# Kernel tuning notes

Hardware: AMD Instinct MI355X
Metric: run time of the kernel (lower is better)

## Reference

```python
import jax, jax.numpy as jnp
import numpy as np

TOP_K = 2


def setup_inputs() -> dict:
    key = jax.random.key(0)
    ks = jax.random.split(key, 6)
    B, S, D, H, E = 2, 2048, 1024, 4096, 8
    s_in = 1.0 / np.sqrt(D)
    s_hid = 1.0 / np.sqrt(H)
    return {
        "x": jax.random.normal(ks[0], (B, S, D), jnp.float32),
        "Wg": jax.random.normal(ks[1], (E, D), jnp.float32) * s_in,
        "W1": jax.random.normal(ks[2], (E, D, H), jnp.float32) * s_in,
        "b1": jax.random.normal(ks[3], (E, H), jnp.float32) * 0.01,
        "W2": jax.random.normal(ks[4], (E, H, D), jnp.float32) * s_hid,
        "b2": jax.random.normal(ks[5], (E, D), jnp.float32) * 0.01,
    }


def reference(x, Wg, W1, b1, W2, b2):
    B, S, D = x.shape
    E = Wg.shape[0]
    T = B * S
    xf = x.reshape(T, D)

    # ---- router ----
    logits = xf @ Wg.T                              # (T, E)
    probs = jax.nn.softmax(logits, axis=-1)
    top_v, top_i = jax.lax.top_k(probs, TOP_K)      # (T, k)
    top_v = top_v / top_v.sum(axis=-1, keepdims=True)

    # aux load-balancing loss
    expert_mask = jax.nn.one_hot(top_i, E, dtype=probs.dtype).sum(axis=1)  # (T, E)
    f = expert_mask.mean(axis=0)
    p = probs.mean(axis=0)
    aux_loss = E * (f * p).sum()

    # ---- combine weights: scatter normalized top-k probs into (T, E) ----
    w = jnp.zeros((T, E), probs.dtype).at[jnp.arange(T)[:, None], top_i].add(top_v)

    # ---- all-expert FFN (grouped GEMM form), weighted combine ----
    h = jax.nn.silu(jnp.einsum('td,edh->teh', xf, W1) + b1[None])   # (T, E, H)
    y = jnp.einsum('teh,ehd->ted', h, W2) + b2[None]                # (T, E, D)
    out = jnp.einsum('ted,te->td', y, w)                            # (T, D)
    return out.reshape(B, S, D), aux_loss
```

## Files before the change

kernel.cpp:

```cpp
#include <hip/hip_runtime.h>
#include <cstdint>
#include <cstddef>

#define T_TOK 4096
#define DIM   1024
#define HID   4096
#define NE    8
#define PAD   128
#define PADMAX 9216
#define KSPLIT2 2

typedef _Float16 half_t;
typedef __attribute__((ext_vector_type(8))) _Float16 half8;
typedef __attribute__((ext_vector_type(4))) float floatx4;

__device__ __forceinline__ float silu_f(float v) {
  return v / (1.0f + expf(-v));
}

__device__ __forceinline__ half8 cvt44(float4 a, float4 b) {
  half8 o;
  o[0] = (half_t)a.x; o[1] = (half_t)a.y; o[2] = (half_t)a.z; o[3] = (half_t)a.w;
  o[4] = (half_t)b.x; o[5] = (half_t)b.y; o[6] = (half_t)b.z; o[7] = (half_t)b.w;
  return o;
}

__device__ __forceinline__ void gload16(const void* g, void* l) {
  __builtin_amdgcn_global_load_lds(
      (const __attribute__((address_space(1))) unsigned int*)g,
      (__attribute__((address_space(3))) unsigned int*)l, 16, 0, 0);
}

__device__ __forceinline__ int xcd_swz(int lin, int Nw) {
  int q = Nw >> 3;
  return (lin & 7) * q + (lin >> 3);
}


__device__ __forceinline__ void write_tiled(const half_t* sT, half_t* dstTile, int tid) {
#pragma unroll
  for (int t2 = 0; t2 < 4; ++t2) {
    int o = (t2 * 256 + tid) * 8;
    int m = o >> 9, p2 = o & 511;
    int lane2 = p2 >> 3;
    int rg = ((m >> 2) << 1) | ((m >> 1) & 1);
    int khalf = m & 1;
    int fr = rg * 16 + (lane2 & 15);
    int fk = khalf * 32 + (lane2 >> 4) * 8;
    half8 v;
#pragma unroll
    for (int j = 0; j < 8; ++j) v[j] = sT[(fk + j) * 136 + fr];
    *(half8*)(dstTile + o) = v;
  }
}

__global__ void k_reset(float* prob_sum, unsigned* cnt, unsigned* cursor,
                        int* pair_tok, float* pair_wt) {
  int i = blockIdx.x * 256 + threadIdx.x;
  if (i < PADMAX) { pair_tok[i] = 0; pair_wt[i] = 0.0f; }
  if (i < NE) { prob_sum[i] = 0.0f; cnt[i] = 0u; cursor[i] = 0u; }
}

__global__ __launch_bounds__(256) void k_cvt_x(const float* __restrict__ x,
                                               half_t* __restrict__ xh) {
  size_t i = (size_t)blockIdx.x * 256 + threadIdx.x;
  const float4* s = (const float4*)(x + i * 8);
  float4 a = s[0], b = s[1];
  *(half8*)(xh + i * 8) = cvt44(a, b);
}

__global__ __launch_bounds__(256) void k_tr_w1(const float* __restrict__ W1,
                                               half_t* __restrict__ W1c,
                                               int j0, int Hc) {
  __shared__ half_t sT[64 * 136];
  int e = blockIdx.z, J = blockIdx.x, Kd = blockIdx.y;
  int tid = threadIdx.x;
  {
    int rr = tid >> 2, q = tid & 3;
    const float* s = W1 + ((size_t)e * DIM + Kd * 64 + rr) * HID + j0 + J * 128 + q * 32;
    float4 f[8];
#pragma unroll
    for (int i = 0; i < 8; ++i) f[i] = ((const float4*)s)[i];
    half_t* d = sT + rr * 136 + q * 32;
#pragma unroll
    for (int i = 0; i < 4; ++i) *(half8*)(d + i * 8) = cvt44(f[2 * i], f[2 * i + 1]);
  }
  __syncthreads();
  half_t* dstTile = W1c + (((size_t)e * (Hc >> 7) + J) * (DIM / 64) + Kd) * 8192;
  write_tiled(sT, dstTile, tid);
}

__global__ __launch_bounds__(256) void k_tr_w2(const float* __restrict__ W2,
                                               half_t* __restrict__ W2c,
                                               int j0, int Hc) {
  __shared__ half_t sT[64 * 136];
  int e = blockIdx.z, J = blockIdx.x, K2 = blockIdx.y;
  int tid = threadIdx.x;
  {
    int hh = tid >> 2, q = tid & 3;
    const float* s = W2 + ((size_t)e * HID + j0 + K2 * 64 + hh) * DIM + J * 128 + q * 32;
    float4 f[8];
#pragma unroll
    for (int i = 0; i < 8; ++i) f[i] = ((const float4*)s)[i];
    half_t* d = sT + hh * 136 + q * 32;
#pragma unroll
    for (int i = 0; i < 4; ++i) *(half8*)(d + i * 8) = cvt44(f[2 * i], f[2 * i + 1]);
  }
  __syncthreads();
  half_t* dstTile = W2c + (((size_t)e * (DIM / 128) + J) * (Hc >> 6) + K2) * 8192;
  write_tiled(sT, dstTile, tid);
}

__global__ __launch_bounds__(256) void k_router(
    const float* __restrict__ x, const float* __restrict__ Wg,
    int* __restrict__ top_i, float* __restrict__ top_w,
    float* __restrict__ prob_sum, unsigned* __restrict__ cnt) {
  __shared__ float sWg[NE * DIM];
  __shared__ float sProb[NE];
  __shared__ unsigned sCnt[NE];
  int tid = threadIdx.x;
  if (tid < NE) { sProb[tid] = 0.0f; sCnt[tid] = 0u; }
  for (int i = tid; i < NE * DIM; i += 256) sWg[i] = Wg[i];
  __syncthreads();

  int wave = tid >> 6, lane = tid & 63;
  for (int it = 0; it < 4; ++it) {
    int t = blockIdx.x * 16 + wave * 4 + it;
    const float* xp = x + (size_t)t * DIM;
    float acc[NE];
#pragma unroll
    for (int e = 0; e < NE; ++e) acc[e] = 0.0f;
    for (int i = 0; i < DIM / 64; ++i) {
      int d = i * 64 + lane;
      float xd = xp[d];
#pragma unroll
      for (int e = 0; e < NE; ++e) acc[e] = fmaf(xd, sWg[e * DIM + d], acc[e]);
    }
#pragma unroll
    for (int off = 32; off > 0; off >>= 1)
#pragma unroll
      for (int e = 0; e < NE; ++e) acc[e] += __shfl_xor(acc[e], off, 64);

    if (lane == 0) {
      float m = acc[0];
#pragma unroll
      for (int e = 1; e < NE; ++e) m = fmaxf(m, acc[e]);
      float pr[NE]; float s = 0.0f;
#pragma unroll
      for (int e = 0; e < NE; ++e) { pr[e] = expf(acc[e] - m); s += pr[e]; }
      float inv = 1.0f / s;
#pragma unroll
      for (int e = 0; e < NE; ++e) pr[e] *= inv;
      int i0 = 0; float v0 = pr[0];
#pragma unroll
      for (int e = 1; e < NE; ++e) if (pr[e] > v0) { v0 = pr[e]; i0 = e; }
      int i1 = -1; float v1 = -1.0f;
#pragma unroll
      for (int e = 0; e < NE; ++e) if (e != i0 && pr[e] > v1) { v1 = pr[e]; i1 = e; }
      float wn = 1.0f / (v0 + v1);
      top_i[t * 2 + 0] = i0; top_i[t * 2 + 1] = i1;
      top_w[t * 2 + 0] = v0 * wn; top_w[t * 2 + 1] = v1 * wn;
#pragma unroll
      for (int e = 0; e < NE; ++e) atomicAdd(&sProb[e], pr[e]);
      atomicAdd(&sCnt[i0], 1u);
      atomicAdd(&sCnt[i1], 1u);
    }
  }
  __syncthreads();
  if (tid < NE) {
    atomicAdd(&prob_sum[tid], sProb[tid]);
    atomicAdd(&cnt[tid], sCnt[tid]);
  }
}

__global__ void k_scan(const unsigned* __restrict__ cnt,
                       const float* __restrict__ prob_sum,
                       int* __restrict__ pad_off, int* __restrict__ ptotal,
                       float* __restrict__ aux_out) {
  if (threadIdx.x == 0 && blockIdx.x == 0) {
    int off = 0; float aux = 0.0f;
    for (int e = 0; e < NE; ++e) {
      pad_off[e] = off;
      off += (int)((cnt[e] + (PAD - 1u)) & ~(unsigned)(PAD - 1));
      aux += ((float)cnt[e] / (float)T_TOK) * (prob_sum[e] / (float)T_TOK);
    }
    pad_off[NE] = off;
    *ptotal = off;
    *aux_out = (float)NE * aux;
  }
}

__global__ void k_scatter(const int* __restrict__ top_i, const float* __restrict__ top_w,
                          const int* __restrict__ pad_off, unsigned* __restrict__ cursor,
                          int* __restrict__ pair_tok, float* __restrict__ pair_wt) {
  int t = blockIdx.x * 256 + threadIdx.x;
  if (t >= T_TOK) return;
#pragma unroll
  for (int k = 0; k < 2; ++k) {
    int e = top_i[t * 2 + k];
    unsigned pos = atomicAdd(&cursor[e], 1u);
    int idx = pad_off[e] + (int)pos;
    pair_tok[idx] = t;
    pair_wt[idx]  = top_w[t * 2 + k];
  }
}

__global__ void k_init_out(const int* __restrict__ top_i, const float* __restrict__ top_w,
                           const float* __restrict__ b2, float* __restrict__ out) {
  int idx = blockIdx.x * 256 + threadIdx.x;
  int t = idx >> 10, d = idx & (DIM - 1);
  int e0 = top_i[t * 2 + 0], e1 = top_i[t * 2 + 1];
  out[idx] = top_w[t * 2 + 0] * b2[e0 * DIM + d] + top_w[t * 2 + 1] * b2[e1 * DIM + d];
}

__global__ __launch_bounds__(256) void k_gemm1_a(
    const half_t* __restrict__ xh, const half_t* __restrict__ W1c,
    const float* __restrict__ b1, const int* __restrict__ pair_tok,
    const int* __restrict__ pad_off, const int* __restrict__ ptotal,
    half_t* __restrict__ hbuf, int j0, int Hc) {
  __shared__ half_t lds[16384];
  int wid = xcd_swz(blockIdx.x, gridDim.x);
  int col = wid / (PADMAX / 128);
  int row = wid % (PADMAX / 128);
  int P = *ptotal;
  int p0 = row * 128;
  if (p0 >= P) return;
  int e = 0;
#pragma unroll
  for (int q = 1; q < NE; ++q) if (p0 >= pad_off[q]) e = q;

  int tid = threadIdx.x, w = tid >> 6, l = tid & 63;
  int lr = l & 15, lq = l >> 4;
  int wr = w >> 1, wc = w & 1;
  int w4 = 4 * w;
  int jt = col * 128;

  int tok0 = pair_tok[p0 + (2 * w) * 16 + lr];
  int tok1 = pair_tok[p0 + (2 * w + 1) * 16 + lr];
  const half_t* gA0 = xh + (size_t)tok0 * DIM + lq * 8;
  const half_t* gA1 = xh + (size_t)tok1 * DIM + lq * 8;
  const half_t* gBt = W1c + (((size_t)e * (Hc >> 7) + (jt >> 7)) * (DIM / 64)) * 8192 + l * 8;

  half_t* ldsA = lds;
  half_t* ldsB = lds + 8192;
  half_t* dA = ldsA + w4 * 512;
  half_t* dB = ldsB + w4 * 512;

  floatx4 acc[4][4];
#pragma unroll
  for (int i = 0; i < 4; ++i)
#pragma unroll
    for (int j = 0; j < 4; ++j) acc[i][j] = (floatx4){0.f, 0.f, 0.f, 0.f};

  for (int s = 0; s < DIM / 64; ++s) {
    int kt = s * 64;
    __syncthreads();
    gload16(gA0 + kt,      dA + 0 * 512);
    gload16(gA0 + kt + 32, dA + 1 * 512);
    gload16(gA1 + kt,      dA + 2 * 512);
    gload16(gA1 + kt + 32, dA + 3 * 512);
    const half_t* gBs = gBt + (size_t)s * 8192;
#pragma unroll
    for (int i = 0; i < 4; ++i) gload16(gBs + (w4 + i) * 512, dB + i * 512);
    __syncthreads();
#pragma unroll
    for (int ks = 0; ks < 2; ++ks) {
      half8 a[4], b[4];
#pragma unroll
      for (int i = 0; i < 4; ++i)
        a[i] = *(const half8*)(ldsA + ((4 * wr + i) * 2 + ks) * 512 + l * 8);
#pragma unroll
      for (int j = 0; j < 4; ++j)
        b[j] = *(const half8*)(ldsB + ((4 * wc + j) * 2 + ks) * 512 + l * 8);
#pragma unroll
      for (int i = 0; i < 4; ++i)
#pragma unroll
        for (int j = 0; j < 4; ++j)
          acc[i][j] = __builtin_amdgcn_mfma_f32_16x16x32_f16(a[i], b[j], acc[i][j], 0, 0, 0);
    }
  }
  __syncthreads();

#pragma unroll
  for (int j = 0; j < 4; ++j) {
    int coll = (4 * wc + j) * 16 + lr;
    float bias = b1[(size_t)e * HID + j0 + jt + coll];
#pragma unroll
    for (int i = 0; i < 4; ++i)
#pragma unroll
      for (int r = 0; r < 4; ++r) {
        int row2 = (4 * wr + i) * 16 + lq * 4 + r;
        lds[row2 * 128 + coll] = (half_t)silu_f(acc[i][j][r] + bias);
      }
  }
  __syncthreads();
  {
    size_t tb = ((size_t)(p0 >> 7) * (Hc >> 6) + (jt >> 6)) * 8192;
#pragma unroll
    for (int t2 = 0; t2 < 8; ++t2) {
      int o = (t2 * 256 + tid) * 8;
      int kk = o >> 13, rem = o & 8191;
      int m = rem >> 9, p2 = rem & 511;
      int lane2 = p2 >> 3;
      int rg = ((m >> 2) << 1) | ((m >> 1) & 1);
      int rr = rg * 16 + (lane2 & 15);
      int colb = kk * 64 + (m & 1) * 32 + (lane2 >> 4) * 8;
      *(half8*)(hbuf + tb + o) = *(const half8*)(lds + rr * 128 + colb);
    }
  }
}

__global__ __launch_bounds__(256) void k_gemm2_a(
    const half_t* __restrict__ hbuf, const half_t* __restrict__ W2c,
    const int* __restrict__ pair_tok, const float* __restrict__ pair_wt,
    const int* __restrict__ pad_off, const int* __restrict__ ptotal,
    float* __restrict__ out, int Hc) {
  __shared__ half_t lds[16384];
  int wid = xcd_swz(blockIdx.x, gridDim.x);
  int c  = wid & 7;
  int rz = wid >> 3;
  int row = rz % (PADMAX / 128);
  int zk  = rz / (PADMAX / 128);
  int P = *ptotal;
  int p0 = row * 128;
  if (p0 >= P) return;
  int e = 0;
#pragma unroll
  for (int q = 1; q < NE; ++q) if (p0 >= pad_off[q]) e = q;

  int tid = threadIdx.x, w = tid >> 6, l = tid & 63;
  int lr = l & 15, lq = l >> 4;
  int wr = w >> 1, wc = w & 1;
  int w4 = 4 * w;
  int jt = c * 128;

  int nkt = Hc >> 6;
  int t_beg = (zk * nkt) / KSPLIT2;
  int t_end = ((zk + 1) * nkt) / KSPLIT2;

  const half_t* gA = hbuf + ((size_t)row * nkt) * 8192 + l * 8;
  const half_t* gB = W2c + (((size_t)e * (DIM / 128) + c) * nkt) * 8192 + l * 8;

  half_t* ldsA = lds;
  half_t* ldsB = lds + 8192;
  half_t* dA = ldsA + w4 * 512;
  half_t* dB = ldsB + w4 * 512;

  floatx4 acc[4][4];
#pragma unroll
  for (int i = 0; i < 4; ++i)
#pragma unroll
    for (int j = 0; j < 4; ++j) acc[i][j] = (floatx4){0.f, 0.f, 0.f, 0.f};

  for (int s = t_beg; s < t_end; ++s) {
    const half_t* gAs = gA + (size_t)s * 8192;
    const half_t* gBs = gB + (size_t)s * 8192;
    __syncthreads();
#pragma unroll
    for (int i = 0; i < 4; ++i) gload16(gAs + (w4 + i) * 512, dA + i * 512);
#pragma unroll
    for (int i = 0; i < 4; ++i) gload16(gBs + (w4 + i) * 512, dB + i * 512);
    __syncthreads();
#pragma unroll
    for (int ks = 0; ks < 2; ++ks) {
      half8 a[4], b[4];
#pragma unroll
      for (int i = 0; i < 4; ++i)
        a[i] = *(const half8*)(ldsA + ((4 * wr + i) * 2 + ks) * 512 + l * 8);
#pragma unroll
      for (int j = 0; j < 4; ++j)
        b[j] = *(const half8*)(ldsB + ((4 * wc + j) * 2 + ks) * 512 + l * 8);
#pragma unroll
      for (int i = 0; i < 4; ++i)
#pragma unroll
        for (int j = 0; j < 4; ++j)
          acc[i][j] = __builtin_amdgcn_mfma_f32_16x16x32_f16(a[i], b[j], acc[i][j], 0, 0, 0);
    }
  }

#pragma unroll
  for (int i = 0; i < 4; ++i)
#pragma unroll
    for (int r = 0; r < 4; ++r) {
      int row2 = (4 * wr + i) * 16 + lq * 4 + r;
      float wt = pair_wt[p0 + row2];
      if (wt != 0.0f) {
        int tok = pair_tok[p0 + row2];
        float* op = out + (size_t)tok * DIM + jt;
#pragma unroll
        for (int j = 0; j < 4; ++j) {
          int coll = (4 * wc + j) * 16 + lr;
          unsafeAtomicAdd(op + coll, wt * acc[i][j][r]);
        }
      }
    }
}

__global__ __launch_bounds__(256) void k_gemm1_b(
    const half_t* __restrict__ xh, const float* __restrict__ W1,
    const float* __restrict__ b1, const int* __restrict__ pair_tok,
    const int* __restrict__ pad_off, const int* __restrict__ ptotal,
    half_t* __restrict__ hout, int j0, int Hc) {
  __shared__ half_t lds[16384];
  int P = *ptotal;
  int p0 = blockIdx.y * 128;
  if (p0 >= P) return;
  int e = 0;
#pragma unroll
  for (int q = 1; q < NE; ++q) if (p0 >= pad_off[q]) e = q;

  int tid = threadIdx.x, w = tid >> 6, l = tid & 63;
  int lr = l & 15, lq = l >> 4;
  int wr = w >> 1, wc = w & 1;
  int jt = blockIdx.x * 128;

  int tok0 = pair_tok[p0 + (2 * w) * 16 + lr];
  int tok1 = pair_tok[p0 + (2 * w + 1) * 16 + lr];
  const half_t* gA0 = xh + (size_t)tok0 * DIM + lq * 8;
  const half_t* gA1 = xh + (size_t)tok1 * DIM + lq * 8;
  const float* gBb = W1 + (size_t)e * DIM * HID + j0 + jt;
  const float* gB0 = gBb + (2 * w) * 16 + lr;
  const float* gB1 = gBb + (2 * w + 1) * 16 + lr;

  half_t* ldsA = lds;
  half_t* ldsB = lds + 8192;

  floatx4 acc[4][4];
#pragma unroll
  for (int i = 0; i < 4; ++i)
#pragma unroll
    for (int j = 0; j < 4; ++j) acc[i][j] = (floatx4){0.f, 0.f, 0.f, 0.f};

  for (int kt = 0; kt < DIM; kt += 64) {
    half8 va0 = *(const half8*)(gA0 + kt);
    half8 va1 = *(const half8*)(gA0 + kt + 32);
    half8 va2 = *(const half8*)(gA1 + kt);
    half8 va3 = *(const half8*)(gA1 + kt + 32);
    half8 vb[4];
#pragma unroll
    for (int fg = 0; fg < 4; ++fg) {
      const float* gb = (fg >> 1) ? gB1 : gB0;
      int kbase = kt + (fg & 1) * 32 + lq * 8;
#pragma unroll
      for (int j = 0; j < 8; ++j)
        vb[fg][j] = (half_t)gb[(size_t)(kbase + j) * HID];
    }
    __syncthreads();
    *(half8*)(ldsA + (4 * w + 0) * 512 + l * 8) = va0;
    *(half8*)(ldsA + (4 * w + 1) * 512 + l * 8) = va1;
    *(half8*)(ldsA + (4 * w + 2) * 512 + l * 8) = va2;
    *(half8*)(ldsA + (4 * w + 3) * 512 + l * 8) = va3;
    *(half8*)(ldsB + (4 * w + 0) * 512 + l * 8) = vb[0];
    *(half8*)(ldsB + (4 * w + 1) * 512 + l * 8) = vb[1];
    *(half8*)(ldsB + (4 * w + 2) * 512 + l * 8) = vb[2];
    *(half8*)(ldsB + (4 * w + 3) * 512 + l * 8) = vb[3];
    __syncthreads();
#pragma unroll
    for (int ks = 0; ks < 2; ++ks) {
      half8 a[4], b[4];
#pragma unroll
      for (int i = 0; i < 4; ++i)
        a[i] = *(const half8*)(ldsA + ((4 * wr + i) * 2 + ks) * 512 + l * 8);
#pragma unroll
      for (int j = 0; j < 4; ++j)
        b[j] = *(const half8*)(ldsB + ((4 * wc + j) * 2 + ks) * 512 + l * 8);
#pragma unroll
      for (int i = 0; i < 4; ++i)
#pragma unroll
        for (int j = 0; j < 4; ++j)
          acc[i][j] = __builtin_amdgcn_mfma_f32_16x16x32_f16(a[i], b[j], acc[i][j], 0, 0, 0);
    }
  }
  __syncthreads();

#pragma unroll
  for (int j = 0; j < 4; ++j) {
    int coll = (4 * wc + j) * 16 + lr;
    float bias = b1[(size_t)e * HID + j0 + jt + coll];
#pragma unroll
    for (int i = 0; i < 4; ++i)
#pragma unroll
      for (int r = 0; r < 4; ++r) {
        int row = (4 * wr + i) * 16 + lq * 4 + r;
        lds[row * 128 + coll] = (half_t)silu_f(acc[i][j][r] + bias);
      }
  }
  __syncthreads();
#pragma unroll
  for (int ps = 0; ps < 4; ++ps) {
    int r = ps * 32 + (tid >> 3), c = (tid & 7) * 16;
    half8 v0 = *(const half8*)(lds + r * 128 + c);
    half8 v1 = *(const half8*)(lds + r * 128 + c + 8);
    half_t* dst = hout + (size_t)(p0 + r) * Hc + jt + c;
    *(half8*)dst = v0;
    *(half8*)(dst + 8) = v1;
  }
}

__global__ __launch_bounds__(256) void k_gemm2_b(
    const half_t* __restrict__ hbuf, const float* __restrict__ W2,
    const int* __restrict__ pair_tok, const float* __restrict__ pair_wt,
    const int* __restrict__ pad_off, const int* __restrict__ ptotal,
    float* __restrict__ out, int j0, int Hc) {
  __shared__ half_t lds[16384];
  int P = *ptotal;
  int p0 = blockIdx.y * 128;
  if (p0 >= P) return;
  int e = 0;
#pragma unroll
  for (int q = 1; q < NE; ++q) if (p0 >= pad_off[q]) e = q;

  int tid = threadIdx.x, w = tid >> 6, l = tid & 63;
  int lr = l & 15, lq = l >> 4;
  int wr = w >> 1, wc = w & 1;
  int jt = blockIdx.x * 128;

  const half_t* gA0 = hbuf + (size_t)(p0 + (2 * w) * 16 + lr) * Hc + lq * 8;
  const half_t* gA1 = hbuf + (size_t)(p0 + (2 * w + 1) * 16 + lr) * Hc + lq * 8;
  const float* gBb = W2 + (size_t)e * HID * DIM + jt;
  const float* gB0 = gBb + (2 * w) * 16 + lr;
  const float* gB1 = gBb + (2 * w + 1) * 16 + lr;

  half_t* ldsA = lds;
  half_t* ldsB = lds + 8192;

  floatx4 acc[4][4];
#pragma unroll
  for (int i = 0; i < 4; ++i)
#pragma unroll
    for (int j = 0; j < 4; ++j) acc[i][j] = (floatx4){0.f, 0.f, 0.f, 0.f};

  for (int kt = 0; kt < Hc; kt += 64) {
    half8 va0 = *(const half8*)(gA0 + kt);
    half8 va1 = *(const half8*)(gA0 + kt + 32);
    half8 va2 = *(const half8*)(gA1 + kt);
    half8 va3 = *(const half8*)(gA1 + kt + 32);
    half8 vb[4];
#pragma unroll
    for (int fg = 0; fg < 4; ++fg) {
      const float* gb = (fg >> 1) ? gB1 : gB0;
      int kbase = j0 + kt + (fg & 1) * 32 + lq * 8;
#pragma unroll
      for (int j = 0; j < 8; ++j)
        vb[fg][j] = (half_t)gb[(size_t)(kbase + j) * DIM];
    }
    __syncthreads();
    *(half8*)(ldsA + (4 * w + 0) * 512 + l * 8) = va0;
    *(half8*)(ldsA + (4 * w + 1) * 512 + l * 8) = va1;
    *(half8*)(ldsA + (4 * w + 2) * 512 + l * 8) = va2;
    *(half8*)(ldsA + (4 * w + 3) * 512 + l * 8) = va3;
    *(half8*)(ldsB + (4 * w + 0) * 512 + l * 8) = vb[0];
    *(half8*)(ldsB + (4 * w + 1) * 512 + l * 8) = vb[1];
    *(half8*)(ldsB + (4 * w + 2) * 512 + l * 8) = vb[2];
    *(half8*)(ldsB + (4 * w + 3) * 512 + l * 8) = vb[3];
    __syncthreads();
#pragma unroll
    for (int ks = 0; ks < 2; ++ks) {
      half8 a[4], b[4];
#pragma unroll
      for (int i = 0; i < 4; ++i)
        a[i] = *(const half8*)(ldsA + ((4 * wr + i) * 2 + ks) * 512 + l * 8);
#pragma unroll
      for (int j = 0; j < 4; ++j)
        b[j] = *(const half8*)(ldsB + ((4 * wc + j) * 2 + ks) * 512 + l * 8);
#pragma unroll
      for (int i = 0; i < 4; ++i)
#pragma unroll
        for (int j = 0; j < 4; ++j)
          acc[i][j] = __builtin_amdgcn_mfma_f32_16x16x32_f16(a[i], b[j], acc[i][j], 0, 0, 0);
    }
  }

#pragma unroll
  for (int i = 0; i < 4; ++i)
#pragma unroll
    for (int r = 0; r < 4; ++r) {
      int row = (4 * wr + i) * 16 + lq * 4 + r;
      float wt = pair_wt[p0 + row];
      if (wt != 0.0f) {
        int tok = pair_tok[p0 + row];
        float* op = out + (size_t)tok * DIM + jt;
#pragma unroll
        for (int j = 0; j < 4; ++j) {
          int coll = (4 * wc + j) * 16 + lr;
          unsafeAtomicAdd(op + coll, wt * acc[i][j][r]);
        }
      }
    }
}

extern "C" void kernel_launch(void* const* d_in, const int* in_sizes, int n_in,
                              void* d_out, int out_size, void* d_ws, size_t ws_size,
                              hipStream_t stream) {
  const float* x  = (const float*)d_in[0];
  const float* Wg = (const float*)d_in[1];
  const float* W1 = (const float*)d_in[2];
  const float* b1 = (const float*)d_in[3];
  const float* W2 = (const float*)d_in[4];
  const float* b2 = (const float*)d_in[5];
  float* out = (float*)d_out;

  char* p = (char*)d_ws;
  auto alloc = [&](size_t bytes) -> char* {
    char* r = p; p += (bytes + 255) & ~(size_t)255; return r;
  };
  int*      top_i    = (int*)     alloc((size_t)T_TOK * 2 * sizeof(int));
  float*    top_w    = (float*)   alloc((size_t)T_TOK * 2 * sizeof(float));
  float*    prob_sum = (float*)   alloc(NE * sizeof(float));
  unsigned* cnt      = (unsigned*)alloc(NE * sizeof(unsigned));
  int*      pad_off  = (int*)     alloc((NE + 1) * sizeof(int));
  int*      ptotal   = (int*)     alloc(sizeof(int));
  unsigned* cursor   = (unsigned*)alloc(NE * sizeof(unsigned));
  int*      pair_tok = (int*)     alloc(PADMAX * sizeof(int));
  float*    pair_wt  = (float*)   alloc(PADMAX * sizeof(float));
  half_t*   xh       = (half_t*)  alloc((size_t)T_TOK * DIM * sizeof(half_t));

  size_t used  = (size_t)(p - (char*)d_ws);
  size_t avail = ws_size > used ? ws_size - used : 0;

  size_t per_col_a = (size_t)2 * NE * DIM * sizeof(half_t) + (size_t)PADMAX * sizeof(half_t);
  int HcA = (int)((avail / per_col_a) & ~(size_t)127);
  if (HcA > HID) HcA = HID;
  bool modeA = (HcA >= 128);

  k_reset<<<dim3((PADMAX + 255) / 256), 256, 0, stream>>>(prob_sum, cnt, cursor, pair_tok, pair_wt);
  k_cvt_x<<<dim3((size_t)T_TOK * DIM / 8 / 256), 256, 0, stream>>>(x, xh);
  k_router<<<dim3(T_TOK / 16), 256, 0, stream>>>(x, Wg, top_i, top_w, prob_sum, cnt);
  k_scan<<<1, 64, 0, stream>>>(cnt, prob_sum, pad_off, ptotal, out + (size_t)T_TOK * DIM);
  k_scatter<<<dim3(T_TOK / 256), 256, 0, stream>>>(top_i, top_w, pad_off, cursor, pair_tok, pair_wt);
  k_init_out<<<dim3((size_t)T_TOK * DIM / 256), 256, 0, stream>>>(top_i, top_w, b2, out);

  if (modeA) {
    int Hc = HcA;
    half_t* W1c  = (half_t*)alloc((size_t)NE * Hc * DIM * sizeof(half_t));
    half_t* W2c  = (half_t*)alloc((size_t)NE * DIM * Hc * sizeof(half_t));
    half_t* hbuf = (half_t*)alloc((size_t)PADMAX * Hc * sizeof(half_t));
    for (int jb = 0; jb < HID; jb += Hc) {
      int hc = (HID - jb) < Hc ? (HID - jb) : Hc;
      k_tr_w1<<<dim3(hc / 128, DIM / 64, NE), 256, 0, stream>>>(W1, W1c, jb, hc);
      k_gemm1_a<<<dim3((hc / 128) * (PADMAX / 128)), 256, 0, stream>>>(
          xh, W1c, b1, pair_tok, pad_off, ptotal, hbuf, jb, hc);
      k_tr_w2<<<dim3(DIM / 128, hc / 64, NE), 256, 0, stream>>>(W2, W2c, jb, hc);
      k_gemm2_a<<<dim3((DIM / 128) * (PADMAX / 128) * KSPLIT2), 256, 0, stream>>>(
          hbuf, W2c, pair_tok, pair_wt, pad_off, ptotal, out, hc);
    }
  } else {
    int Hc = (int)((avail / ((size_t)PADMAX * sizeof(half_t))) & ~(size_t)127);
    if (Hc > HID) Hc = HID;
    if (Hc < 128) Hc = 128;
    half_t* hbuf = (half_t*)alloc((size_t)PADMAX * Hc * sizeof(half_t));
    for (int jb = 0; jb < HID; jb += Hc) {
      int hc = (HID - jb) < Hc ? (HID - jb) : Hc;
      k_gemm1_b<<<dim3(hc / 128, PADMAX / 128), 256, 0, stream>>>(
          xh, W1, b1, pair_tok, pad_off, ptotal, hbuf, jb, hc);
      k_gemm2_b<<<dim3(DIM / 128, PADMAX / 128), 256, 0, stream>>>(
          hbuf, W2, pair_tok, pair_wt, pad_off, ptotal, out, jb, hc);
    }
  }
}
```

Measured before the change: 626.3 us.

## Double-buffer LDS tiles in both expert GEMM kernels

Both grouped GEMM kernels now use two LDS buffers per operand. The global-to-LDS load for the next K step is issued before computing on the current buffer, so each step needs one barrier instead of two. The goal is to hide global load latency behind the MFMA work. In exchange, LDS per block doubles to 64 KB, which can cut the number of resident blocks per CU.

```diff
diff --git a/kernel.cpp b/kernel.cpp
--- a/kernel.cpp
+++ b/kernel.cpp
@@ -218,7 +218,7 @@
     const float* __restrict__ b1, const int* __restrict__ pair_tok,
     const int* __restrict__ pad_off, const int* __restrict__ ptotal,
     half_t* __restrict__ hbuf, int j0, int Hc) {
-  __shared__ half_t lds[16384];
+  __shared__ half_t lds[32768];
   int wid = xcd_swz(blockIdx.x, gridDim.x);
   int col = wid / (PADMAX / 128);
   int row = wid % (PADMAX / 128);
@@ -241,10 +241,10 @@
   const half_t* gA1 = xh + (size_t)tok1 * DIM + lq * 8;
   const half_t* gBt = W1c + (((size_t)e * (Hc >> 7) + (jt >> 7)) * (DIM / 64)) * 8192 + l * 8;
 
-  half_t* ldsA = lds;
-  half_t* ldsB = lds + 8192;
-  half_t* dA = ldsA + w4 * 512;
-  half_t* dB = ldsB + w4 * 512;
+  half_t* A0 = lds;
+  half_t* B0 = lds + 8192;
+  half_t* A1 = lds + 16384;
+  half_t* B1 = lds + 24576;
 
   floatx4 acc[4][4];
 #pragma unroll
@@ -252,32 +252,43 @@
 #pragma unroll
     for (int j = 0; j < 4; ++j) acc[i][j] = (floatx4){0.f, 0.f, 0.f, 0.f};
 
-  for (int s = 0; s < DIM / 64; ++s) {
+  auto STAGE = [&](int s, half_t* bA, half_t* bB) {
     int kt = s * 64;
-    __syncthreads();
-    gload16(gA0 + kt,      dA + 0 * 512);
-    gload16(gA0 + kt + 32, dA + 1 * 512);
-    gload16(gA1 + kt,      dA + 2 * 512);
-    gload16(gA1 + kt + 32, dA + 3 * 512);
+    gload16(gA0 + kt,      bA + (w4 + 0) * 512);
+    gload16(gA0 + kt + 32, bA + (w4 + 1) * 512);
+    gload16(gA1 + kt,      bA + (w4 + 2) * 512);
+    gload16(gA1 + kt + 32, bA + (w4 + 3) * 512);
     const half_t* gBs = gBt + (size_t)s * 8192;
 #pragma unroll
-    for (int i = 0; i < 4; ++i) gload16(gBs + (w4 + i) * 512, dB + i * 512);
-    __syncthreads();
+    for (int i = 0; i < 4; ++i) gload16(gBs + (w4 + i) * 512, bB + (w4 + i) * 512);
+  };
+  auto COMP = [&](const half_t* bA, const half_t* bB) {
 #pragma unroll
     for (int ks = 0; ks < 2; ++ks) {
       half8 a[4], b[4];
 #pragma unroll
       for (int i = 0; i < 4; ++i)
-        a[i] = *(const half8*)(ldsA + ((4 * wr + i) * 2 + ks) * 512 + l * 8);
+        a[i] = *(const half8*)(bA + ((4 * wr + i) * 2 + ks) * 512 + l * 8);
 #pragma unroll
       for (int j = 0; j < 4; ++j)
-        b[j] = *(const half8*)(ldsB + ((4 * wc + j) * 2 + ks) * 512 + l * 8);
+        b[j] = *(const half8*)(bB + ((4 * wc + j) * 2 + ks) * 512 + l * 8);
 #pragma unroll
       for (int i = 0; i < 4; ++i)
 #pragma unroll
         for (int j = 0; j < 4; ++j)
           acc[i][j] = __builtin_amdgcn_mfma_f32_16x16x32_f16(a[i], b[j], acc[i][j], 0, 0, 0);
     }
+  };
+
+  STAGE(0, A0, B0);
+#pragma unroll 1
+  for (int s = 0; s < DIM / 64; s += 2) {
+    __syncthreads();
+    if (s + 1 < DIM / 64) STAGE(s + 1, A1, B1);
+    COMP(A0, B0);
+    __syncthreads();
+    if (s + 2 < DIM / 64) STAGE(s + 2, A0, B0);
+    COMP(A1, B1);
   }
   __syncthreads();
 
@@ -315,7 +326,7 @@
     const int* __restrict__ pair_tok, const float* __restrict__ pair_wt,
     const int* __restrict__ pad_off, const int* __restrict__ ptotal,
     float* __restrict__ out, int Hc) {
-  __shared__ half_t lds[16384];
+  __shared__ half_t lds[32768];
   int wid = xcd_swz(blockIdx.x, gridDim.x);
   int c  = wid & 7;
   int rz = wid >> 3;
@@ -341,10 +352,10 @@
   const half_t* gA = hbuf + ((size_t)row * nkt) * 8192 + l * 8;
   const half_t* gB = W2c + (((size_t)e * (DIM / 128) + c) * nkt) * 8192 + l * 8;
 
-  half_t* ldsA = lds;
-  half_t* ldsB = lds + 8192;
-  half_t* dA = ldsA + w4 * 512;
-  half_t* dB = ldsB + w4 * 512;
+  half_t* A0 = lds;
+  half_t* B0 = lds + 8192;
+  half_t* A1 = lds + 16384;
+  half_t* B1 = lds + 24576;
 
   floatx4 acc[4][4];
 #pragma unroll
@@ -352,30 +363,45 @@
 #pragma unroll
     for (int j = 0; j < 4; ++j) acc[i][j] = (floatx4){0.f, 0.f, 0.f, 0.f};
 
-  for (int s = t_beg; s < t_end; ++s) {
+  auto STAGE = [&](int s, half_t* bA, half_t* bB) {
     const half_t* gAs = gA + (size_t)s * 8192;
     const half_t* gBs = gB + (size_t)s * 8192;
-    __syncthreads();
-#pragma unroll
-    for (int i = 0; i < 4; ++i) gload16(gAs + (w4 + i) * 512, dA + i * 512);
-#pragma unroll
-    for (int i = 0; i < 4; ++i) gload16(gBs + (w4 + i) * 512, dB + i * 512);
-    __syncthreads();
+#pragma unroll
+    for (int i = 0; i < 4; ++i) gload16(gAs + (w4 + i) * 512, bA + (w4 + i) * 512);
+#pragma unroll
+    for (int i = 0; i < 4; ++i) gload16(gBs + (w4 + i) * 512, bB + (w4 + i) * 512);
+  };
+  auto COMP = [&](const half_t* bA, const half_t* bB) {
 #pragma unroll
     for (int ks = 0; ks < 2; ++ks) {
       half8 a[4], b[4];
 #pragma unroll
       for (int i = 0; i < 4; ++i)
-        a[i] = *(const half8*)(ldsA + ((4 * wr + i) * 2 + ks) * 512 + l * 8);
+        a[i] = *(const half8*)(bA + ((4 * wr + i) * 2 + ks) * 512 + l * 8);
 #pragma unroll
       for (int j = 0; j < 4; ++j)
-        b[j] = *(const half8*)(ldsB + ((4 * wc + j) * 2 + ks) * 512 + l * 8);
+        b[j] = *(const half8*)(bB + ((4 * wc + j) * 2 + ks) * 512 + l * 8);
 #pragma unroll
       for (int i = 0; i < 4; ++i)
 #pragma unroll
         for (int j = 0; j < 4; ++j)
           acc[i][j] = __builtin_amdgcn_mfma_f32_16x16x32_f16(a[i], b[j], acc[i][j], 0, 0, 0);
     }
+  };
+
+  int s = t_beg;
+  STAGE(s, A0, B0);
+#pragma unroll 1
+  while (true) {
+    __syncthreads();
+    if (s + 1 < t_end) STAGE(s + 1, A1, B1);
+    COMP(A0, B0);
+    if (s + 1 >= t_end) break;
+    __syncthreads();
+    if (s + 2 < t_end) STAGE(s + 2, A0, B0);
+    COMP(A1, B1);
+    s += 2;
+    if (s >= t_end) break;
   }
 
 #pragma unroll
```

After: 643.8 us. 2.8% more time.
